# Kernel optimization log

Measured on AMD Instinct MI355X. Metric: run time of the kernel, lower is better.

## Reference

```python
import jax, jax.numpy as jnp
import numpy as np

B, P, O, C = 64, 8732, 32, 81
IMG = 224.0
THRESH = 0.5
NEG_POS = 3.0
ALPHA = 1.0


def cxcy_to_xy(b):
    return jnp.concatenate([b[..., :2] - b[..., 2:] / 2, b[..., :2] + b[..., 2:] / 2], -1)


def xy_to_cxcy(b):
    return jnp.concatenate([(b[..., :2] + b[..., 2:]) / 2, b[..., 2:] - b[..., :2]], -1)


def coco_to_xy(b):  # [x, y, w, h] -> [xmin, ymin, xmax, ymax]
    return jnp.concatenate([b[..., :2], b[..., :2] + b[..., 2:]], -1)


def cxcy_to_gcxgcy(cxcy, priors):  # SSD offset encoding, variances 10 / 5
    g_cxcy = (cxcy[..., :2] - priors[..., :2]) / (priors[..., 2:] / 10.0)
    g_wh = jnp.log(cxcy[..., 2:] / priors[..., 2:]) * 5.0
    return jnp.concatenate([g_cxcy, g_wh], -1)


def pairwise_iou(a, b):  # a: [O,4] xy, b: [P,4] xy -> [O,P]
    lt = jnp.maximum(a[:, None, :2], b[None, :, :2])
    rb = jnp.minimum(a[:, None, 2:], b[None, :, 2:])
    wh = jnp.clip(rb - lt, 0.0)
    inter = wh[..., 0] * wh[..., 1]
    area_a = (a[:, 2] - a[:, 0]) * (a[:, 3] - a[:, 1])
    area_b = (b[:, 2] - b[:, 0]) * (b[:, 3] - b[:, 1])
    return inter / (area_a[:, None] + area_b[None, :] - inter)


def setup_inputs() -> dict:
    key = jax.random.key(0)
    k1, k2, k3, k4, k5, k6, k7 = jax.random.split(key, 7)
    pred_locs = jax.random.normal(k1, (B, P, 4), dtype=jnp.float32)
    pred_scores = jax.random.normal(k2, (B, P, C), dtype=jnp.float32)
    # COCO-format gt boxes [x, y, w, h] in pixel coords, guaranteed inside image
    xy = jax.random.uniform(k3, (B, O, 2), minval=0.0, maxval=IMG * 0.55)
    wh = jax.random.uniform(k4, (B, O, 2), minval=8.0, maxval=IMG * 0.4)
    gt_boxes = jnp.concatenate([xy, wh], -1)
    gt_labels = jax.random.randint(k5, (B, O), 1, C)  # foreground labels 1..C-1
    p_cxcy = jax.random.uniform(k6, (P, 2), minval=0.05, maxval=0.95)
    p_wh = jax.random.uniform(k7, (P, 2), minval=0.05, maxval=0.5)
    priors_cxcy = jnp.concatenate([p_cxcy, p_wh], -1)
    return {"pred_locs": pred_locs, "pred_scores": pred_scores,
            "gt_boxes": gt_boxes, "gt_labels": gt_labels,
            "priors_cxcy": priors_cxcy}


def reference(pred_locs, pred_scores, gt_boxes, gt_labels, priors_cxcy):
    priors_xy = cxcy_to_xy(priors_cxcy)

    def match(boxes_coco, labels):  # one image: [O,4] coco, [O] int
        boxes_xy = coco_to_xy(boxes_coco) / IMG  # normalize to [0,1]
        ov = pairwise_iou(boxes_xy, priors_xy)  # [O, P]
        overlap_for_prior = ov.max(axis=0)       # [P]
        object_for_prior = ov.argmax(axis=0)     # [P]
        prior_for_object = ov.argmax(axis=1)     # [O]
        # force each object to claim its best prior
        object_for_prior = object_for_prior.at[prior_for_object].set(jnp.arange(O))
        overlap_for_prior = overlap_for_prior.at[prior_for_object].set(1.0)
        label_for_prior = labels[object_for_prior]
        label_for_prior = jnp.where(overlap_for_prior < THRESH, 0, label_for_prior)
        true_locs = cxcy_to_gcxgcy(xy_to_cxcy(boxes_xy[object_for_prior]), priors_cxcy)
        return true_locs, label_for_prior

    true_locs, true_classes = jax.vmap(match)(gt_boxes, gt_labels)  # [B,P,4], [B,P]

    positive = true_classes != 0          # [B, P]
    n_pos = positive.sum(axis=1)          # [B]
    n_pos_cl = jnp.maximum(n_pos, 1).astype(jnp.float32)
    n_hard_neg = NEG_POS * n_pos_cl

    # SmoothL1 (beta=1), mean over positive prior coords
    diff = jnp.abs(pred_locs - true_locs)
    sl1 = jnp.where(diff < 1.0, 0.5 * diff * diff, diff - 0.5)  # [B,P,4]
    total_pos = n_pos.sum()
    loc_loss = jnp.where(
        total_pos > 0,
        jnp.where(positive[..., None], sl1, 0.0).sum()
        / jnp.maximum(total_pos * 4, 1).astype(jnp.float32),
        0.0,
    )

    # per-prior cross entropy
    logp = jax.nn.log_softmax(pred_scores, axis=-1)
    ce = -jnp.take_along_axis(logp, true_classes[..., None], axis=-1)[..., 0]  # [B,P]

    conf_pos_sum = jnp.where(positive, ce, 0.0).sum()
    ce_neg = jnp.where(positive, 0.0, ce)
    ce_neg_sorted = -jnp.sort(-ce_neg, axis=1)  # descending per image
    ranks = jnp.arange(P)[None, :]
    hard = ranks < n_hard_neg[:, None]
    conf_hard_neg_sum = jnp.where(hard, ce_neg_sorted, 0.0).sum()

    conf_loss = (conf_hard_neg_sum + conf_pos_sum) / n_pos_cl.sum()
    return conf_loss + ALPHA * loc_loss
```

## Files before the change

### kernel.cpp

```cpp
#include <hip/hip_runtime.h>
#include <cstdint>
#include <cstddef>

#define BB 64
#define PP 8732
#define OO 32
#define CC 81
#define NBM 35
#define NB2 273

__global__ __launch_bounds__(256) void k_match(
    const float* __restrict__ gt_boxes,
    const float4* __restrict__ priors,
    float* __restrict__ ovl, int* __restrict__ obj,
    unsigned long long* __restrict__ part)
{
    int b = blockIdx.y, blk = blockIdx.x;
    int tid = threadIdx.x;
    int p = blk * 256 + tid;
    bool pv = p < PP;
    __shared__ float bx1[OO], by1[OO], bx2[OO], by2[OO], bar[OO];
    __shared__ float mat[OO][264];
    __shared__ unsigned long long po[OO][8];
    if (tid < OO) {
        const float* g = gt_boxes + ((size_t)b * OO + tid) * 4;
        float x1 = g[0] / 224.0f, y1 = g[1] / 224.0f;
        float x2 = (g[0] + g[2]) / 224.0f, y2 = (g[1] + g[3]) / 224.0f;
        bx1[tid] = x1; by1[tid] = y1; bx2[tid] = x2; by2[tid] = y2;
        bar[tid] = (x2 - x1) * (y2 - y1);
    }
    __syncthreads();
    float4 pr = priors[pv ? p : 0];
    float px1 = pr.x - pr.z * 0.5f, py1 = pr.y - pr.w * 0.5f;
    float px2 = pr.x + pr.z * 0.5f, py2 = pr.y + pr.w * 0.5f;
    float parea = (px2 - px1) * (py2 - py1);
    float best = -1.0f; int bo = 0;
    #pragma unroll
    for (int o = 0; o < OO; ++o) {
        float lx = fmaxf(bx1[o], px1), ly = fmaxf(by1[o], py1);
        float rx = fminf(bx2[o], px2), ry = fminf(by2[o], py2);
        float w = fmaxf(rx - lx, 0.0f), h = fmaxf(ry - ly, 0.0f);
        float inter = w * h;
        float iou = inter / (bar[o] + parea - inter);
        iou = pv ? iou : 0.0f;
        mat[o][tid] = iou;
        if (iou > best) { best = iou; bo = o; }
    }
    if (pv) {
        size_t idx = (size_t)b * PP + p;
        ovl[idx] = best;
        obj[idx] = bo;
    }
    __syncthreads();
    {
        int o = tid >> 3, j = tid & 7;
        float bv = -1.0f; int bt = 0;
        #pragma unroll
        for (int k = 0; k < 32; ++k) {
            int t = j + 8 * k;
            float v = mat[o][t];
            if (v > bv) { bv = v; bt = t; }
        }
        unsigned pg = (unsigned)(blk * 256 + bt);
        po[o][j] = ((unsigned long long)__float_as_uint(bv) << 32)
                 | (unsigned long long)(0xFFFFFFFFu - pg);
    }
    __syncthreads();
    if (tid < OO) {
        unsigned long long m = po[tid][0];
        #pragma unroll
        for (int j = 1; j < 8; ++j) if (po[tid][j] > m) m = po[tid][j];
        part[((size_t)b * NBM + blk) * OO + tid] = m;
    }
}

__global__ void k_force(const unsigned long long* __restrict__ part,
                        float* __restrict__ ovl, int* __restrict__ obj)
{
    int b = blockIdx.x;
    __shared__ int s_pfo[OO];
    int t = threadIdx.x;
    if (t < OO) {
        unsigned long long m = part[((size_t)b * NBM + 0) * OO + t];
        for (int blk = 1; blk < NBM; ++blk) {
            unsigned long long v = part[((size_t)b * NBM + blk) * OO + t];
            if (v > m) m = v;
        }
        s_pfo[t] = (int)(0xFFFFFFFFu - (unsigned)(m & 0xFFFFFFFFull));
    }
    __syncthreads();
    if (t == 0) {
        for (int o = 0; o < OO; ++o) {
            int p = s_pfo[o];
            obj[(size_t)b * PP + p] = o;
            ovl[(size_t)b * PP + p] = 1.0f;
        }
    }
}

__global__ __launch_bounds__(256) void k_ce(
    const float* __restrict__ scores,
    const float4* __restrict__ pred_locs,
    const float* __restrict__ gt_boxes,
    const int* __restrict__ gt_labels,
    const float4* __restrict__ priors,
    const float* __restrict__ ovl, const int* __restrict__ obj,
    float* __restrict__ ceneg,
    float* __restrict__ pp_posce, float* __restrict__ pp_sl1,
    int* __restrict__ pp_np)
{
    int b = blockIdx.y;
    int group = threadIdx.x >> 4, lane = threadIdx.x & 15;
    int p0 = blockIdx.x * 32 + group;
    int p1 = p0 + 16;
    bool v0 = p0 < PP, v1 = p1 < PP;
    size_t i0 = (size_t)b * PP + (size_t)(v0 ? p0 : 0);
    size_t i1 = (size_t)b * PP + (size_t)(v1 ? p1 : 0);
    __shared__ float s_posce, s_sl1;
    __shared__ int s_np;
    if (threadIdx.x == 0) { s_posce = 0.f; s_sl1 = 0.f; s_np = 0; }
    __syncthreads();
    int lab0 = 0, ob0 = 0, lab1 = 0, ob1 = 0;
    if (v0) { float ov = ovl[i0]; ob0 = obj[i0]; lab0 = (ov < 0.5f) ? 0 : gt_labels[b * OO + ob0]; }
    if (v1) { float ov = ovl[i1]; ob1 = obj[i1]; lab1 = (ov < 0.5f) ? 0 : gt_labels[b * OO + ob1]; }
    const float* r0 = scores + i0 * CC;
    const float* r1 = scores + i1 * CC;
    float a0[6], a1[6];
    #pragma unroll
    for (int k = 0; k < 6; ++k) {
        int c = lane + 16 * k;
        bool cv = c < CC;
        a0[k] = (v0 && cv) ? r0[c] : -INFINITY;
        a1[k] = (v1 && cv) ? r1[c] : -INFINITY;
    }
    float se0 = 0.f, xl0 = 0.f, se1 = 0.f, xl1 = 0.f;
    #pragma unroll
    for (int k = 0; k < 6; ++k) {
        int c = lane + 16 * k;
        if (c < CC) {
            se0 += __expf(a0[k]); if (c == lab0) xl0 = a0[k];
            se1 += __expf(a1[k]); if (c == lab1) xl1 = a1[k];
        }
    }
    #pragma unroll
    for (int s = 8; s >= 1; s >>= 1) {
        se0 += __shfl_xor(se0, s, 16);
        xl0 += __shfl_xor(xl0, s, 16);
        se1 += __shfl_xor(se1, s, 16);
        xl1 += __shfl_xor(xl1, s, 16);
    }
    if (lane == 0) {
        #pragma unroll
        for (int pass = 0; pass < 2; ++pass) {
            bool vv = pass ? v1 : v0;
            if (!vv) continue;
            size_t idx = pass ? i1 : i0;
            int lab = pass ? lab1 : lab0;
            int ob  = pass ? ob1 : ob0;
            int p   = pass ? p1 : p0;
            float se = pass ? se1 : se0;
            float xl = pass ? xl1 : xl0;
            float ce = fmaxf(__logf(se) - xl, 0.0f);
            float cn = ce;
            if (lab != 0) {
                cn = 0.f;
                float4 pl = pred_locs[idx];
                float4 pq = priors[p];
                const float* g = gt_boxes + ((size_t)b * OO + ob) * 4;
                float x1 = g[0] / 224.0f, y1 = g[1] / 224.0f;
                float x2 = (g[0] + g[2]) / 224.0f, y2 = (g[1] + g[3]) / 224.0f;
                float cx = (x1 + x2) * 0.5f, cy = (y1 + y2) * 0.5f;
                float w = x2 - x1, h = y2 - y1;
                float tx = (cx - pq.x) / (pq.z / 10.0f);
                float ty = (cy - pq.y) / (pq.w / 10.0f);
                float tw = __logf(w / pq.z) * 5.0f;
                float th = __logf(h / pq.w) * 5.0f;
                float d0 = fabsf(pl.x - tx), d1 = fabsf(pl.y - ty);
                float d2 = fabsf(pl.z - tw), d3 = fabsf(pl.w - th);
                float sl = (d0 < 1.f ? 0.5f * d0 * d0 : d0 - 0.5f)
                         + (d1 < 1.f ? 0.5f * d1 * d1 : d1 - 0.5f)
                         + (d2 < 1.f ? 0.5f * d2 * d2 : d2 - 0.5f)
                         + (d3 < 1.f ? 0.5f * d3 * d3 : d3 - 0.5f);
                atomicAdd(&s_posce, ce);
                atomicAdd(&s_sl1, sl);
                atomicAdd(&s_np, 1);
            }
            ceneg[idx] = cn;
        }
    }
    __syncthreads();
    if (threadIdx.x == 0) {
        int slot = b * NB2 + blockIdx.x;
        pp_posce[slot] = s_posce;
        pp_sl1[slot]   = s_sl1;
        pp_np[slot]    = s_np;
    }
}

__global__ __launch_bounds__(512) void k_topk(
    const float* __restrict__ ceneg,
    const float* __restrict__ pp_posce, const float* __restrict__ pp_sl1,
    const int* __restrict__ pp_np,
    float* __restrict__ hard, float* __restrict__ posce_b,
    float* __restrict__ sl1_b, int* __restrict__ n_pos)
{
    int b = blockIdx.x, tid = threadIdx.x;
    __shared__ float4 sv4[PP / 4];
    __shared__ int s_i[8];
    __shared__ float s_f[8], s_f2[8];
    __shared__ int s_bcast;
    float pc = 0.f, sl = 0.f; int np = 0;
    for (int i = tid; i < NB2; i += 512) {
        pc += pp_posce[b * NB2 + i];
        sl += pp_sl1[b * NB2 + i];
        np += pp_np[b * NB2 + i];
    }
    #pragma unroll
    for (int s = 32; s >= 1; s >>= 1) {
        pc += __shfl_xor(pc, s, 64);
        sl += __shfl_xor(sl, s, 64);
        np += __shfl_xor(np, s, 64);
    }
    int wid = tid >> 6;
    if ((tid & 63) == 0) { s_i[wid] = np; s_f[wid] = pc; s_f2[wid] = sl; }
    const float4* src = (const float4*)(ceneg + (size_t)b * PP);
    for (int i = tid; i < PP / 4; i += 512) sv4[i] = src[i];
    __syncthreads();
    if (tid == 0) {
        int n = 0; float fp = 0.f, fs = 0.f;
        #pragma unroll
        for (int k = 0; k < 8; ++k) { n += s_i[k]; fp += s_f[k]; fs += s_f2[k]; }
        n_pos[b] = n; posce_b[b] = fp; sl1_b[b] = fs;
        s_bcast = n;
    }
    __syncthreads();
    np = s_bcast;
    int K = 3 * (np > 1 ? np : 1);
    if (K > PP) K = PP;
    unsigned lo = 0u, hi = 0x7F800000u;
    while (hi - lo > 1u) {
        unsigned mid = (lo + hi) >> 1;
        float t = __uint_as_float(mid);
        int c = 0;
        for (int i = tid; i < PP / 4; i += 512) {
            float4 q = sv4[i];
            c += (q.x >= t) + (q.y >= t) + (q.z >= t) + (q.w >= t);
        }
        #pragma unroll
        for (int s = 32; s >= 1; s >>= 1) c += __shfl_xor(c, s, 64);
        if ((tid & 63) == 0) s_i[wid] = c;
        __syncthreads();
        if (tid == 0) {
            int n = 0;
            #pragma unroll
            for (int k = 0; k < 8; ++k) n += s_i[k];
            s_bcast = n;
        }
        __syncthreads();
        int cnt = s_bcast;
        if (cnt >= K) lo = mid; else hi = mid;
        __syncthreads();
    }
    float vk = __uint_as_float(lo);
    float sm = 0.f; int cg = 0;
    for (int i = tid; i < PP / 4; i += 512) {
        float4 q = sv4[i];
        if (q.x > vk) { sm += q.x; cg++; }
        if (q.y > vk) { sm += q.y; cg++; }
        if (q.z > vk) { sm += q.z; cg++; }
        if (q.w > vk) { sm += q.w; cg++; }
    }
    #pragma unroll
    for (int s = 32; s >= 1; s >>= 1) {
        sm += __shfl_xor(sm, s, 64);
        cg += __shfl_xor(cg, s, 64);
    }
    if ((tid & 63) == 0) { s_f[wid] = sm; s_i[wid] = cg; }
    __syncthreads();
    if (tid == 0) {
        float S = 0.f; int CG = 0;
        #pragma unroll
        for (int k = 0; k < 8; ++k) { S += s_f[k]; CG += s_i[k]; }
        hard[b] = S + (float)(K - CG) * vk;
    }
}

__global__ void k_final(const int* __restrict__ n_pos, const float* __restrict__ hard,
                        const float* __restrict__ posce_b, const float* __restrict__ sl1_b,
                        float* __restrict__ out)
{
    int t = threadIdx.x;
    int np = (t < BB) ? n_pos[t] : 0;
    float h  = (t < BB) ? hard[t] : 0.f;
    float pc = (t < BB) ? posce_b[t] : 0.f;
    float sl = (t < BB) ? sl1_b[t] : 0.f;
    float cl = (t < BB) ? (float)(np > 1 ? np : 1) : 0.f;
    int tp = np; float hs = h; float cls = cl;
    #pragma unroll
    for (int s = 32; s >= 1; s >>= 1) {
        tp  += __shfl_xor(tp, s, 64);
        hs  += __shfl_xor(hs, s, 64);
        cls += __shfl_xor(cls, s, 64);
        pc  += __shfl_xor(pc, s, 64);
        sl  += __shfl_xor(sl, s, 64);
    }
    if (t == 0) {
        float conf = (hs + pc) / cls;
        float loc = 0.f;
        if (tp > 0) {
            int den = tp * 4; if (den < 1) den = 1;
            loc = sl / (float)den;
        }
        out[0] = conf + loc;
    }
}

extern "C" void kernel_launch(void* const* d_in, const int* in_sizes, int n_in,
                              void* d_out, int out_size, void* d_ws, size_t ws_size,
                              hipStream_t stream)
{
    const float* pred_locs   = (const float*)d_in[0];
    const float* pred_scores = (const float*)d_in[1];
    const float* gt_boxes    = (const float*)d_in[2];
    const int*   gt_labels   = (const int*)d_in[3];
    const float* priors      = (const float*)d_in[4];

    char* ws = (char*)d_ws;
    const size_t npf = (size_t)BB * PP;
    size_t off = 0;
    float* ovl   = (float*)(ws + off); off += 4 * npf;
    int*   obj   = (int*)  (ws + off); off += 4 * npf;
    float* ceneg = (float*)(ws + off); off += 4 * npf;
    unsigned long long* part = (unsigned long long*)(ws + off); off += 8 * (size_t)BB * NBM * OO;
    float* pp_posce = (float*)(ws + off); off += 4 * (size_t)BB * NB2;
    float* pp_sl1   = (float*)(ws + off); off += 4 * (size_t)BB * NB2;
    int*   pp_np    = (int*)  (ws + off); off += 4 * (size_t)BB * NB2;
    float* posce_b  = (float*)(ws + off); off += 4 * BB;
    float* sl1_b    = (float*)(ws + off); off += 4 * BB;
    int*   n_pos    = (int*)  (ws + off); off += 4 * BB;
    float* hard     = (float*)(ws + off); off += 4 * BB;

    dim3 gM(NBM, BB);
    k_match<<<gM, 256, 0, stream>>>(gt_boxes, (const float4*)priors, ovl, obj, part);

    k_force<<<BB, 64, 0, stream>>>(part, ovl, obj);

    dim3 gB(NB2, BB);
    k_ce<<<gB, 256, 0, stream>>>(pred_scores, (const float4*)pred_locs, gt_boxes, gt_labels,
                                 (const float4*)priors, ovl, obj, ceneg,
                                 pp_posce, pp_sl1, pp_np);

    k_topk<<<BB, 512, 0, stream>>>(ceneg, pp_posce, pp_sl1, pp_np,
                                   hard, posce_b, sl1_b, n_pos);

    k_final<<<1, 64, 0, stream>>>(n_pos, hard, posce_b, sl1_b, (float*)d_out);
}
```

Measured before the change: 313.8 us.

## Pack label/object into one int, radix-select top-k, fuse final reduction

```diff
diff --git a/kernel.cpp b/kernel.cpp
--- a/kernel.cpp
+++ b/kernel.cpp
@@ -11,8 +11,9 @@
 
 __global__ __launch_bounds__(256) void k_match(
     const float* __restrict__ gt_boxes,
+    const int* __restrict__ gt_labels,
     const float4* __restrict__ priors,
-    float* __restrict__ ovl, int* __restrict__ obj,
+    int* __restrict__ olab,
     unsigned long long* __restrict__ part)
 {
     int b = blockIdx.y, blk = blockIdx.x;
@@ -20,6 +21,7 @@
     int p = blk * 256 + tid;
     bool pv = p < PP;
     __shared__ float bx1[OO], by1[OO], bx2[OO], by2[OO], bar[OO];
+    __shared__ int slab[OO];
     __shared__ float mat[OO][264];
     __shared__ unsigned long long po[OO][8];
     if (tid < OO) {
@@ -28,6 +30,7 @@
         float x2 = (g[0] + g[2]) / 224.0f, y2 = (g[1] + g[3]) / 224.0f;
         bx1[tid] = x1; by1[tid] = y1; bx2[tid] = x2; by2[tid] = y2;
         bar[tid] = (x2 - x1) * (y2 - y1);
+        slab[tid] = gt_labels[b * OO + tid];
     }
     __syncthreads();
     float4 pr = priors[pv ? p : 0];
@@ -47,9 +50,8 @@
         if (iou > best) { best = iou; bo = o; }
     }
     if (pv) {
-        size_t idx = (size_t)b * PP + p;
-        ovl[idx] = best;
-        obj[idx] = bo;
+        int lab = (best < 0.5f) ? 0 : slab[bo];
+        olab[(size_t)b * PP + p] = (lab << 5) | bo;
     }
     __syncthreads();
     {
@@ -75,11 +77,14 @@
 }
 
 __global__ void k_force(const unsigned long long* __restrict__ part,
-                        float* __restrict__ ovl, int* __restrict__ obj)
+                        const int* __restrict__ gt_labels,
+                        int* __restrict__ olab, int* __restrict__ done)
 {
     int b = blockIdx.x;
+    int t = threadIdx.x;
+    if (b == 0 && t == 0) *done = 0;
     __shared__ int s_pfo[OO];
-    int t = threadIdx.x;
+    __shared__ int s_lab[OO];
     if (t < OO) {
         unsigned long long m = part[((size_t)b * NBM + 0) * OO + t];
         for (int blk = 1; blk < NBM; ++blk) {
@@ -87,13 +92,13 @@
             if (v > m) m = v;
         }
         s_pfo[t] = (int)(0xFFFFFFFFu - (unsigned)(m & 0xFFFFFFFFull));
+        s_lab[t] = gt_labels[b * OO + t];
     }
     __syncthreads();
     if (t == 0) {
         for (int o = 0; o < OO; ++o) {
             int p = s_pfo[o];
-            obj[(size_t)b * PP + p] = o;
-            ovl[(size_t)b * PP + p] = 1.0f;
+            olab[(size_t)b * PP + p] = (s_lab[o] << 5) | o;
         }
     }
 }
@@ -102,9 +107,8 @@
     const float* __restrict__ scores,
     const float4* __restrict__ pred_locs,
     const float* __restrict__ gt_boxes,
-    const int* __restrict__ gt_labels,
     const float4* __restrict__ priors,
-    const float* __restrict__ ovl, const int* __restrict__ obj,
+    const int* __restrict__ olab,
     float* __restrict__ ceneg,
     float* __restrict__ pp_posce, float* __restrict__ pp_sl1,
     int* __restrict__ pp_np)
@@ -121,8 +125,8 @@
     if (threadIdx.x == 0) { s_posce = 0.f; s_sl1 = 0.f; s_np = 0; }
     __syncthreads();
     int lab0 = 0, ob0 = 0, lab1 = 0, ob1 = 0;
-    if (v0) { float ov = ovl[i0]; ob0 = obj[i0]; lab0 = (ov < 0.5f) ? 0 : gt_labels[b * OO + ob0]; }
-    if (v1) { float ov = ovl[i1]; ob1 = obj[i1]; lab1 = (ov < 0.5f) ? 0 : gt_labels[b * OO + ob1]; }
+    if (v0) { int v = olab[i0]; ob0 = v & 31; lab0 = v >> 5; }
+    if (v1) { int v = olab[i1]; ob1 = v & 31; lab1 = v >> 5; }
     const float* r0 = scores + i0 * CC;
     const float* r1 = scores + i1 * CC;
     float a0[6], a1[6];
@@ -202,13 +206,19 @@
     const float* __restrict__ pp_posce, const float* __restrict__ pp_sl1,
     const int* __restrict__ pp_np,
     float* __restrict__ hard, float* __restrict__ posce_b,
-    float* __restrict__ sl1_b, int* __restrict__ n_pos)
+    float* __restrict__ sl1_b, int* __restrict__ n_pos,
+    int* __restrict__ done, float* __restrict__ out)
 {
     int b = blockIdx.x, tid = threadIdx.x;
     __shared__ float4 sv4[PP / 4];
+    __shared__ int hist[8][256];
+    __shared__ int hsum[256];
     __shared__ int s_i[8];
     __shared__ float s_f[8], s_f2[8];
     __shared__ int s_bcast;
+    __shared__ unsigned s_sel;
+    __shared__ int s_krem;
+    __shared__ int s_last;
     float pc = 0.f, sl = 0.f; int np = 0;
     for (int i = tid; i < NB2; i += 512) {
         pc += pp_posce[b * NB2 + i];
@@ -232,36 +242,68 @@
         for (int k = 0; k < 8; ++k) { n += s_i[k]; fp += s_f[k]; fs += s_f2[k]; }
         n_pos[b] = n; posce_b[b] = fp; sl1_b[b] = fs;
         s_bcast = n;
+        int K0 = 3 * (n > 1 ? n : 1);
+        if (K0 > PP) K0 = PP;
+        s_sel = 0u; s_krem = K0;
     }
     __syncthreads();
     np = s_bcast;
     int K = 3 * (np > 1 ? np : 1);
     if (K > PP) K = PP;
-    unsigned lo = 0u, hi = 0x7F800000u;
-    while (hi - lo > 1u) {
-        unsigned mid = (lo + hi) >> 1;
-        float t = __uint_as_float(mid);
-        int c = 0;
+    #pragma unroll
+    for (int s = 24; s >= 0; s -= 8) {
+        for (int i = tid; i < 8 * 256; i += 512) ((int*)hist)[i] = 0;
+        __syncthreads();
+        unsigned pref = s_sel; int krem = s_krem;
+        int hs = s + 8;
+        unsigned prefhi = (hs >= 32) ? 0u : (pref >> (hs & 31));
         for (int i = tid; i < PP / 4; i += 512) {
             float4 q = sv4[i];
-            c += (q.x >= t) + (q.y >= t) + (q.z >= t) + (q.w >= t);
-        }
-        #pragma unroll
-        for (int s = 32; s >= 1; s >>= 1) c += __shfl_xor(c, s, 64);
-        if ((tid & 63) == 0) s_i[wid] = c;
+            float vals[4] = {q.x, q.y, q.z, q.w};
+            #pragma unroll
+            for (int c4 = 0; c4 < 4; ++c4) {
+                unsigned bts = __float_as_uint(vals[c4]);
+                bool ok = (hs >= 32) || ((bts >> (hs & 31)) == prefhi);
+                if (ok) atomicAdd(&hist[wid][(bts >> s) & 255], 1);
+            }
+        }
         __syncthreads();
-        if (tid == 0) {
-            int n = 0;
+        if (tid < 256) {
+            int t = 0;
             #pragma unroll
-            for (int k = 0; k < 8; ++k) n += s_i[k];
-            s_bcast = n;
+            for (int k = 0; k < 8; ++k) t += hist[k][tid];
+            hsum[tid] = t;
         }
         __syncthreads();
-        int cnt = s_bcast;
-        if (cnt >= K) lo = mid; else hi = mid;
+        if (tid < 64) {
+            int lane = tid;
+            int cum = 0;
+            for (int c = 3; c >= 0; --c) {
+                int h = hsum[c * 64 + lane];
+                int suff = h;
+                #pragma unroll
+                for (int off = 1; off < 64; off <<= 1) {
+                    int t = __shfl_down(suff, off);
+                    if (lane + off < 64) suff += t;
+                }
+                int ctot = __shfl(suff, 0);
+                if (cum + ctot >= krem) {
+                    unsigned long long m = __ballot(cum + suff >= krem);
+                    int l = 63 - __builtin_clzll(m);
+                    int suffl = __shfl(suff, l);
+                    int hl = __shfl(h, l);
+                    if (lane == 0) {
+                        s_sel = pref | ((unsigned)(c * 64 + l) << s);
+                        s_krem = krem - (cum + suffl - hl);
+                    }
+                    break;
+                }
+                cum += ctot;
+            }
+        }
         __syncthreads();
     }
-    float vk = __uint_as_float(lo);
+    float vk = __uint_as_float(s_sel);
     float sm = 0.f; int cg = 0;
     for (int i = tid; i < PP / 4; i += 512) {
         float4 q = sv4[i];
@@ -283,35 +325,35 @@
         for (int k = 0; k < 8; ++k) { S += s_f[k]; CG += s_i[k]; }
         hard[b] = S + (float)(K - CG) * vk;
     }
-}
-
-__global__ void k_final(const int* __restrict__ n_pos, const float* __restrict__ hard,
-                        const float* __restrict__ posce_b, const float* __restrict__ sl1_b,
-                        float* __restrict__ out)
-{
-    int t = threadIdx.x;
-    int np = (t < BB) ? n_pos[t] : 0;
-    float h  = (t < BB) ? hard[t] : 0.f;
-    float pc = (t < BB) ? posce_b[t] : 0.f;
-    float sl = (t < BB) ? sl1_b[t] : 0.f;
-    float cl = (t < BB) ? (float)(np > 1 ? np : 1) : 0.f;
-    int tp = np; float hs = h; float cls = cl;
-    #pragma unroll
-    for (int s = 32; s >= 1; s >>= 1) {
-        tp  += __shfl_xor(tp, s, 64);
-        hs  += __shfl_xor(hs, s, 64);
-        cls += __shfl_xor(cls, s, 64);
-        pc  += __shfl_xor(pc, s, 64);
-        sl  += __shfl_xor(sl, s, 64);
-    }
-    if (t == 0) {
-        float conf = (hs + pc) / cls;
-        float loc = 0.f;
-        if (tp > 0) {
-            int den = tp * 4; if (den < 1) den = 1;
-            loc = sl / (float)den;
-        }
-        out[0] = conf + loc;
+    __threadfence();
+    if (tid == 0) s_last = (atomicAdd(done, 1) == BB - 1) ? 1 : 0;
+    __syncthreads();
+    if (s_last) {
+        __threadfence();
+        if (tid < 64) {
+            int t = tid;
+            int np2 = n_pos[t];
+            float h2 = hard[t], pc2 = posce_b[t], sl2 = sl1_b[t];
+            float cl = (float)(np2 > 1 ? np2 : 1);
+            int tp = np2; float hs2 = h2; float cls = cl;
+            #pragma unroll
+            for (int sft = 32; sft >= 1; sft >>= 1) {
+                tp  += __shfl_xor(tp, sft, 64);
+                hs2 += __shfl_xor(hs2, sft, 64);
+                cls += __shfl_xor(cls, sft, 64);
+                pc2 += __shfl_xor(pc2, sft, 64);
+                sl2 += __shfl_xor(sl2, sft, 64);
+            }
+            if (t == 0) {
+                float conf = (hs2 + pc2) / cls;
+                float loc = 0.f;
+                if (tp > 0) {
+                    int den = tp * 4; if (den < 1) den = 1;
+                    loc = sl2 / (float)den;
+                }
+                out[0] = conf + loc;
+            }
+        }
     }
 }
 
@@ -328,8 +370,7 @@
     char* ws = (char*)d_ws;
     const size_t npf = (size_t)BB * PP;
     size_t off = 0;
-    float* ovl   = (float*)(ws + off); off += 4 * npf;
-    int*   obj   = (int*)  (ws + off); off += 4 * npf;
+    int*   olab  = (int*)  (ws + off); off += 4 * npf;
     float* ceneg = (float*)(ws + off); off += 4 * npf;
     unsigned long long* part = (unsigned long long*)(ws + off); off += 8 * (size_t)BB * NBM * OO;
     float* pp_posce = (float*)(ws + off); off += 4 * (size_t)BB * NB2;
@@ -339,19 +380,18 @@
     float* sl1_b    = (float*)(ws + off); off += 4 * BB;
     int*   n_pos    = (int*)  (ws + off); off += 4 * BB;
     float* hard     = (float*)(ws + off); off += 4 * BB;
+    int*   done     = (int*)  (ws + off); off += 4;
 
     dim3 gM(NBM, BB);
-    k_match<<<gM, 256, 0, stream>>>(gt_boxes, (const float4*)priors, ovl, obj, part);
-
-    k_force<<<BB, 64, 0, stream>>>(part, ovl, obj);
+    k_match<<<gM, 256, 0, stream>>>(gt_boxes, gt_labels, (const float4*)priors, olab, part);
+
+    k_force<<<BB, 64, 0, stream>>>(part, gt_labels, olab, done);
 
     dim3 gB(NB2, BB);
-    k_ce<<<gB, 256, 0, stream>>>(pred_scores, (const float4*)pred_locs, gt_boxes, gt_labels,
-                                 (const float4*)priors, ovl, obj, ceneg,
+    k_ce<<<gB, 256, 0, stream>>>(pred_scores, (const float4*)pred_locs, gt_boxes,
+                                 (const float4*)priors, olab, ceneg,
                                  pp_posce, pp_sl1, pp_np);
 
     k_topk<<<BB, 512, 0, stream>>>(ceneg, pp_posce, pp_sl1, pp_np,
-                                   hard, posce_b, sl1_b, n_pos);
-
-    k_final<<<1, 64, 0, stream>>>(n_pos, hard, posce_b, sl1_b, (float*)d_out);
-}
+                                   hard, posce_b, sl1_b, n_pos, done, (float*)d_out);
+}
```

After: 315.0 us. About the same (+0.4%).
